# Optimization experiments

Measured on AMD Instinct MI355X. Metric: run time of the kernel, lower is better.

The kernel has to match this reference:

```python
import jax, jax.numpy as jnp
import numpy as np

N_NODES = 50000
N_EDGES = 500000
HID = 256
LAYERS = 15
IN_CH = 2
EPS = 1e-5


def setup_inputs() -> dict:
    key = jax.random.key(0)
    ks = jax.random.split(key, 16)
    s = 0.02
    x = jax.random.normal(ks[0], (N_NODES, IN_CH), dtype=jnp.float32)
    edge_index = jax.random.randint(ks[1], (2, N_EDGES), 0, N_NODES, dtype=jnp.int32)
    # torch-style Linear weights: [out_features, in_features]
    W_in = jax.random.normal(ks[2], (HID, IN_CH), dtype=jnp.float32) * s
    Wrel = jax.random.normal(ks[3], (LAYERS, HID, HID), dtype=jnp.float32) * s
    brel = jnp.zeros((LAYERS, HID), dtype=jnp.float32)
    Wroot = jax.random.normal(ks[4], (LAYERS, HID, HID), dtype=jnp.float32) * s
    gamma = jnp.ones((LAYERS, HID), dtype=jnp.float32)
    beta = jnp.zeros((LAYERS, HID), dtype=jnp.float32)
    W1 = jax.random.normal(ks[5], (HID, 2 * HID), dtype=jnp.float32) * s
    b1 = jnp.zeros((HID,), dtype=jnp.float32)
    W2 = jax.random.normal(ks[6], (HID, HID), dtype=jnp.float32) * s
    b2 = jnp.zeros((HID,), dtype=jnp.float32)
    W3 = jax.random.normal(ks[7], (1, HID), dtype=jnp.float32) * s
    b3 = jnp.zeros((1,), dtype=jnp.float32)
    return {"x": x, "edge_index": edge_index, "W_in": W_in, "Wrel": Wrel,
            "brel": brel, "Wroot": Wroot, "gamma": gamma, "beta": beta,
            "W1": W1, "b1": b1, "W2": W2, "b2": b2, "W3": W3, "b3": b3}


def reference(x, edge_index, W_in, Wrel, brel, Wroot, gamma, beta,
              W1, b1, W2, b2, W3, b3):
    n = x.shape[0]
    src, dst = edge_index[0], edge_index[1]
    h = x @ W_in.T  # input_fc, no bias -> [N, HID]

    def layer(carry, p):
        Wr, br, Wo, g, bt = p
        # GraphConv (aggr='add'): lin_rel(sum_j x_j) + lin_root(x_i)
        agg = jax.ops.segment_sum(carry[src], dst, num_segments=n)
        out = agg @ Wr.T + br + carry @ Wo.T
        # BatchNorm1d, training-mode batch stats (biased var)
        mean = out.mean(axis=0)
        var = out.var(axis=0)
        out = (out - mean) * jax.lax.rsqrt(var + EPS) * g + bt
        return carry + jax.nn.relu(out), None

    h, _ = jax.lax.scan(layer, h, (Wrel, brel, Wroot, gamma, beta))

    # edge MLP on cat([x[row], x[col]])
    e = jnp.concatenate([h[src], h[dst]], axis=-1)  # [E, 2*HID]
    z = jax.nn.relu(e @ W1.T + b1)
    z = jax.nn.relu(z @ W2.T + b2)
    return jax.nn.sigmoid(z @ W3.T + b3)  # [E, 1]
```

## Files before the change

### kernel.cpp

```cpp
#include <hip/hip_runtime.h>
#include <hip/hip_fp8.h>
#include <cstdint>
#include <cstddef>

#define HID 256

typedef __bf16 bf16;
typedef __bf16 bf16x4 __attribute__((ext_vector_type(4)));
typedef __bf16 bf16x8 __attribute__((ext_vector_type(8)));
typedef float f32x4 __attribute__((ext_vector_type(4)));
typedef unsigned char u8;
union f8x8 { uint2 u; u8 b[8]; };

__device__ inline u8 to_fp8(float v) {
  __hip_fp8_e4m3 t(v);
  return t.__x;
}
__device__ inline float from_fp8(u8 b) {
  __hip_fp8_e4m3 t;
  t.__x = b;
  return (float)t;
}


__global__ void k_zero_i32(int* __restrict__ p, int n) {
  int i = blockIdx.x * blockDim.x + threadIdx.x;
  if (i < n) p[i] = 0;
}

__global__ void k_hist(const int* __restrict__ ei, int* __restrict__ deg, int E) {
  int i = blockIdx.x * blockDim.x + threadIdx.x;
  if (i < E) atomicAdd(&deg[ei[E + i]], 1);
}

__global__ void k_scan1(const int* __restrict__ deg, int* __restrict__ offs,
                        int* __restrict__ bsums, int n) {
  __shared__ int sh[1024];
  int i = blockIdx.x * 1024 + threadIdx.x;
  int v = (i < n) ? deg[i] : 0;
  sh[threadIdx.x] = v;
  __syncthreads();
  for (int d = 1; d < 1024; d <<= 1) {
    int t = (threadIdx.x >= (unsigned)d) ? sh[threadIdx.x - d] : 0;
    __syncthreads();
    sh[threadIdx.x] += t;
    __syncthreads();
  }
  if (i < n) offs[i] = sh[threadIdx.x] - v;
  if (threadIdx.x == 1023) bsums[blockIdx.x] = sh[1023];
}

__global__ void k_scan2(int* __restrict__ bsums, int nb) {
  if (threadIdx.x == 0 && blockIdx.x == 0) {
    int run = 0;
    for (int b = 0; b < nb; ++b) { int t = bsums[b]; bsums[b] = run; run += t; }
  }
}

__global__ void k_scan3(int* __restrict__ offs, int* __restrict__ cursor,
                        const int* __restrict__ bsums, int n, int E) {
  int i = blockIdx.x * 1024 + threadIdx.x;
  if (i < n) { int o = offs[i] + bsums[blockIdx.x]; offs[i] = o; cursor[i] = o; }
  if (i == 0) offs[n] = E;
}

__global__ void k_fill(const int* __restrict__ ei, int* __restrict__ cursor,
                       int* __restrict__ csr, int* __restrict__ edst,
                       int* __restrict__ eperm, int E) {
  int i = blockIdx.x * blockDim.x + threadIdx.x;
  if (i < E) {
    int s = ei[i], d = ei[E + i];
    int pos = atomicAdd(&cursor[d], 1);
    csr[pos] = s;
    edst[pos] = d;
    eperm[pos] = i;
  }
}


__global__ void k_pack(const float* __restrict__ W, bf16* __restrict__ P,
                       int OUT, int K, int count) {
  int g = blockIdx.x * blockDim.x + threadIdx.x;
  int total = count * OUT * (K >> 3);
  if (g >= total) return;
  int lane = g & 63;
  int rest = g >> 6;
  int KT = K >> 5;
  int kt = rest % KT;
  int rest2 = rest / KT;
  int OT = OUT >> 4;
  int tile = rest2 % OT;
  int mat = rest2 / OT;
  const float* src = W + (size_t)mat * OUT * K +
                     (size_t)(tile * 16 + (lane & 15)) * K + kt * 32 + (lane >> 4) * 8;
  bf16* dst = P + (size_t)g * 8;
#pragma unroll
  for (int j = 0; j < 8; ++j) dst[j] = (bf16)src[j];
}


__global__ __launch_bounds__(256) void k_input_fc(
    const float* __restrict__ x, const float* __restrict__ Win,
    bf16* __restrict__ hb, u8* __restrict__ h8,
    float* __restrict__ sums0, int N) {
  if (blockIdx.x == 0) { sums0[threadIdx.x] = 0.f; sums0[256 + threadIdx.x] = 0.f; }
  int gid = blockIdx.x * blockDim.x + threadIdx.x;
  int total = N * 32;
  int stride = gridDim.x * blockDim.x;
  for (int idx = gid; idx < total; idx += stride) {
    int node = idx >> 5, c8 = idx & 31;
    float xa = x[2 * node], xb = x[2 * node + 1];
    bf16x8 o;
    f8x8 p;
#pragma unroll
    for (int k = 0; k < 8; ++k) {
      int c = c8 * 8 + k;
      float v = xa * Win[2 * c] + xb * Win[2 * c + 1];
      o[k] = (bf16)v;
      p.b[k] = to_fp8(v);
    }
    *(bf16x8*)(hb + (size_t)node * HID + c8 * 8) = o;
    *(uint2*)(h8 + (size_t)node * HID + c8 * 8) = p.u;
  }
}


__global__ __launch_bounds__(256) void k_aggregate(
    const u8* __restrict__ h8, const int* __restrict__ offs,
    const int* __restrict__ csr, bf16* __restrict__ aggb, int N) {
  int gwave = (int)((blockIdx.x * blockDim.x + threadIdx.x) >> 6);
  int lane = threadIdx.x & 63;
  int node = gwave * 2 + (lane >> 5);
  int l32 = lane & 31;
  if (node >= N) return;
  int e0 = offs[node], e1 = offs[node + 1];
  float a[8] = {};
  int e = e0;
  for (; e + 3 < e1; e += 4) {
    int s0 = csr[e], s1 = csr[e + 1], s2 = csr[e + 2], s3 = csr[e + 3];
    f8x8 p0, p1, p2, p3;
    p0.u = *(const uint2*)(h8 + (size_t)s0 * HID + l32 * 8);
    p1.u = *(const uint2*)(h8 + (size_t)s1 * HID + l32 * 8);
    p2.u = *(const uint2*)(h8 + (size_t)s2 * HID + l32 * 8);
    p3.u = *(const uint2*)(h8 + (size_t)s3 * HID + l32 * 8);
#pragma unroll
    for (int k = 0; k < 8; ++k)
      a[k] += (from_fp8(p0.b[k]) + from_fp8(p1.b[k])) +
              (from_fp8(p2.b[k]) + from_fp8(p3.b[k]));
  }
  for (; e < e1; ++e) {
    int s0 = csr[e];
    f8x8 p0;
    p0.u = *(const uint2*)(h8 + (size_t)s0 * HID + l32 * 8);
#pragma unroll
    for (int k = 0; k < 8; ++k) a[k] += from_fp8(p0.b[k]);
  }
  bf16x8 o;
#pragma unroll
  for (int k = 0; k < 8; ++k) o[k] = (bf16)a[k];
  *(bf16x8*)(aggb + (size_t)node * HID + l32 * 8) = o;
}


__global__ __launch_bounds__(256, 2) void k_layer_gemm(
    const bf16* __restrict__ aggb, const bf16* __restrict__ hb,
    const bf16* __restrict__ Pr, const bf16* __restrict__ Po,
    const float* __restrict__ bias, bf16* __restrict__ out,
    float* __restrict__ sums, int N) {
  __shared__ __align__(16) bf16 bt[64 * 64 * 8];
  __shared__ float bsum[256], bsq[256];
  int tid = threadIdx.x;
  int wave = tid >> 6, lane = tid & 63;
  int l15 = lane & 15, lq = lane >> 4;
  int m0 = blockIdx.x * 128;
  f32x4 acc[4][8] = {};
  const bf16* PrW = Pr + (size_t)wave * 4 * 8 * 64 * 8;
  const bf16* PoW = Po + (size_t)wave * 4 * 8 * 64 * 8;
  int row = tid & 127, half = tid >> 7;
  int sj = row >> 4, sl = row & 15;
  int gr = m0 + row;
  bool ok = gr < N;

  for (int phase = 0; phase < 2; ++phase) {
    const bf16* src = phase ? hb : aggb;
    if (phase) __syncthreads();
    {
#pragma unroll
      for (int i2 = 0; i2 < 16; ++i2) {
        int c = half * 16 + i2;
        bf16x8 v = {};
        if (ok) v = *(const bf16x8*)(src + (size_t)gr * HID + c * 8);
        *(bf16x8*)(&bt[(((c >> 2) * 8 + sj) * 64 + (c & 3) * 16 + sl) * 8]) = v;
      }
    }
    __syncthreads();
    const bf16* PW = phase ? PoW : PrW;
    for (int kt = 0; kt < 8; ++kt) {
      bf16x8 bfr[8];
#pragma unroll
      for (int j = 0; j < 8; ++j)
        bfr[j] = *(const bf16x8*)(&bt[((kt * 8 + j) * 64 + lane) * 8]);
#pragma unroll
      for (int i = 0; i < 4; ++i) {
        bf16x8 afr = *(const bf16x8*)(PW + ((size_t)(i * 8 + kt) * 64 + lane) * 8);
#pragma unroll
        for (int j = 0; j < 8; ++j)
          acc[i][j] = __builtin_amdgcn_mfma_f32_16x16x32_bf16(afr, bfr[j], acc[i][j], 0, 0, 0);
      }
    }
  }

  f32x4 bv[4];
#pragma unroll
  for (int i = 0; i < 4; ++i)
    bv[i] = *(const f32x4*)(bias + wave * 64 + i * 16 + lq * 4);
  float s[4][4] = {}, q[4][4] = {};
#pragma unroll
  for (int j = 0; j < 8; ++j) {
    int gn = m0 + j * 16 + l15;
    bool okj = gn < N;
#pragma unroll
    for (int i = 0; i < 4; ++i) {
      bf16x4 o;
#pragma unroll
      for (int r = 0; r < 4; ++r) {
        float v = acc[i][j][r] + bv[i][r];
        o[r] = (bf16)v;
        if (okj) { s[i][r] += v; q[i][r] += v * v; }
      }
      if (okj) *(bf16x4*)(out + (size_t)gn * HID + wave * 64 + i * 16 + lq * 4) = o;
    }
  }
#pragma unroll
  for (int d = 1; d < 16; d <<= 1) {
#pragma unroll
    for (int i = 0; i < 4; ++i)
#pragma unroll
      for (int r = 0; r < 4; ++r) {
        s[i][r] += __shfl_xor(s[i][r], d, 64);
        q[i][r] += __shfl_xor(q[i][r], d, 64);
      }
  }
  if (l15 == 0) {
#pragma unroll
    for (int i = 0; i < 4; ++i)
#pragma unroll
      for (int r = 0; r < 4; ++r) {
        bsum[wave * 64 + i * 16 + lq * 4 + r] = s[i][r];
        bsq[wave * 64 + i * 16 + lq * 4 + r] = q[i][r];
      }
  }
  __syncthreads();
  atomicAdd(&sums[tid], bsum[tid]);
  atomicAdd(&sums[256 + tid], bsq[tid]);
}


__global__ __launch_bounds__(256) void k_bn_residual(
    const bf16* __restrict__ outb, bf16* __restrict__ hb, u8* __restrict__ h8,
    const float* __restrict__ sums, float* __restrict__ zsums,
    const float* __restrict__ gamma, const float* __restrict__ beta,
    int N, float invN) {
  int t = threadIdx.x;
  if (blockIdx.x == 0) { zsums[t] = 0.f; zsums[256 + t] = 0.f; }
  int cg = (t & 31) * 8;
  int r0 = blockIdx.x * 32 + (t >> 5) * 4;
  float a[8], b[8];
#pragma unroll
  for (int k = 0; k < 8; ++k) {
    int c = cg + k;
    float mean = sums[c] * invN;
    float var = sums[256 + c] * invN - mean * mean;
    float istd = rsqrtf(var + 1e-5f);
    a[k] = istd * gamma[c];
    b[k] = fmaf(-mean, a[k], beta[c]);
  }
  int r1 = min(r0 + 4, N);
  for (int r = r0; r < r1; ++r) {
    size_t idx = (size_t)r * HID + cg;
    bf16x8 ov = *(const bf16x8*)(outb + idx);
    bf16x8 hv = *(const bf16x8*)(hb + idx);
    bf16x8 o;
    f8x8 p;
#pragma unroll
    for (int k = 0; k < 8; ++k) {
      float y = fmaf((float)ov[k], a[k], b[k]);
      y = fmaxf(y, 0.f);
      float hn = (float)hv[k] + y;
      o[k] = (bf16)hn;
      p.b[k] = to_fp8(hn);
    }
    *(bf16x8*)(hb + idx) = o;
    *(uint2*)(h8 + idx) = p.u;
  }
}


__global__ __launch_bounds__(256, 2) void k_edge_mlp(
    const bf16* __restrict__ hb, const int* __restrict__ csr,
    const int* __restrict__ edst, const int* __restrict__ eperm,
    const bf16* __restrict__ P1, const float* __restrict__ b1v,
    const bf16* __restrict__ P2, const float* __restrict__ b2v,
    const float* __restrict__ w3, const float* __restrict__ b3,
    float* __restrict__ outp, int E) {
  __shared__ __align__(16) bf16 z1f[64 * 64 * 8];
  __shared__ int nd[256];
  __shared__ int oidx[128];
  __shared__ float red[128];
  int tid = threadIdx.x;
  int e0 = blockIdx.x * 128;
  {
    int p = e0 + (tid & 127);
    if (tid < 128) {
      nd[tid] = (p < E) ? csr[p] : 0;
      oidx[tid] = (p < E) ? eperm[p] : -1;
      red[tid] = 0.f;
    } else {
      nd[tid] = (p < E) ? edst[p] : 0;
    }
  }
  int wave = tid >> 6, lane = tid & 63;
  int l15 = lane & 15, lq = lane >> 4;
  int row = tid & 127, half = tid >> 7;
  int sslotA = ((row >> 4) * 64 + (half * 2) * 16 + (row & 15)) * 8;
  int sslotB = ((row >> 4) * 64 + (half * 2 + 1) * 16 + (row & 15)) * 8;
  __syncthreads();

  int dnode[8];
#pragma unroll
  for (int j = 0; j < 8; ++j) dnode[j] = nd[128 + j * 16 + l15];

  f32x4 acc[4][8] = {};
  const bf16* P1W = P1 + (size_t)wave * 4 * 16 * 64 * 8;
  {
    int node = nd[row];
    const bf16* rp = hb + (size_t)node * HID + half * 16;
    *(bf16x8*)(&z1f[sslotA]) = *(const bf16x8*)(rp);
    *(bf16x8*)(&z1f[sslotB]) = *(const bf16x8*)(rp + 8);
  }
  __syncthreads();
  for (int ks = 0; ks < 8; ++ks) {
    bf16x8 vn0, vn1;
    bool has = (ks + 1) < 8;
    if (has) {
      int node = nd[row];
      const bf16* rp = hb + (size_t)node * HID + (ks + 1) * 32 + half * 16;
      vn0 = *(const bf16x8*)(rp);
      vn1 = *(const bf16x8*)(rp + 8);
    }
    const bf16* cur = z1f + (ks & 1) * 4096;
    bf16x8 bfr[8];
#pragma unroll
    for (int j = 0; j < 8; ++j)
      bfr[j] = *(const bf16x8*)(&cur[(j * 64 + lane) * 8]);
#pragma unroll
    for (int i = 0; i < 4; ++i) {
      bf16x8 wf = *(const bf16x8*)(P1W + ((size_t)(i * 16 + ks) * 64 + lane) * 8);
#pragma unroll
      for (int j = 0; j < 8; ++j)
        acc[i][j] = __builtin_amdgcn_mfma_f32_16x16x32_bf16(wf, bfr[j], acc[i][j], 0, 0, 0);
    }
    if (has) {
      bf16* nxt = z1f + ((ks + 1) & 1) * 4096;
      *(bf16x8*)(&nxt[sslotA]) = vn0;
      *(bf16x8*)(&nxt[sslotB]) = vn1;
    }
    __syncthreads();
  }

  for (int ks2 = 0; ks2 < 8; ++ks2) {
    bf16x8 bfr[8];
#pragma unroll
    for (int j = 0; j < 8; ++j)
      bfr[j] = *(const bf16x8*)(hb + (size_t)dnode[j] * HID + ks2 * 32 + lq * 8);
#pragma unroll
    for (int i = 0; i < 4; ++i) {
      bf16x8 wf = *(const bf16x8*)(P1W + ((size_t)(i * 16 + 8 + ks2) * 64 + lane) * 8);
#pragma unroll
      for (int j = 0; j < 8; ++j)
        acc[i][j] = __builtin_amdgcn_mfma_f32_16x16x32_bf16(wf, bfr[j], acc[i][j], 0, 0, 0);
    }
  }

  {
    f32x4 b1i[4];
#pragma unroll
    for (int i = 0; i < 4; ++i)
      b1i[i] = *(const f32x4*)(b1v + wave * 64 + i * 16 + lq * 4);
#pragma unroll
    for (int j = 0; j < 8; ++j) {
#pragma unroll
      for (int i = 0; i < 4; ++i) {
        bf16x4 o;
#pragma unroll
        for (int r = 0; r < 4; ++r)
          o[r] = (bf16)fmaxf(acc[i][j][r] + b1i[i][r], 0.f);
        int kt = wave * 2 + (i >> 1);
        int slt = l15 + 16 * ((i & 1) * 2 + (lq >> 1));
        *(bf16x4*)(&z1f[((j * 8 + kt) * 64 + slt) * 8 + (lq & 1) * 4]) = o;
      }
    }
  }
  __syncthreads();

  f32x4 acc2[4][8] = {};
  const bf16* P2W = P2 + (size_t)wave * 4 * 8 * 64 * 8;
  for (int ks = 0; ks < 8; ++ks) {
    bf16x8 zf[8];
#pragma unroll
    for (int j = 0; j < 8; ++j)
      zf[j] = *(const bf16x8*)(&z1f[((j * 8 + ks) * 64 + lane) * 8]);
#pragma unroll
    for (int i = 0; i < 4; ++i) {
      bf16x8 wf = *(const bf16x8*)(P2W + ((size_t)(i * 8 + ks) * 64 + lane) * 8);
#pragma unroll
      for (int j = 0; j < 8; ++j)
        acc2[i][j] = __builtin_amdgcn_mfma_f32_16x16x32_bf16(wf, zf[j], acc2[i][j], 0, 0, 0);
    }
  }

  f32x4 b2i[4], w3i[4];
#pragma unroll
  for (int i = 0; i < 4; ++i) {
    b2i[i] = *(const f32x4*)(b2v + wave * 64 + i * 16 + lq * 4);
    w3i[i] = *(const f32x4*)(w3 + wave * 64 + i * 16 + lq * 4);
  }
  float sj2[8] = {};
#pragma unroll
  for (int j = 0; j < 8; ++j)
#pragma unroll
    for (int i = 0; i < 4; ++i)
#pragma unroll
      for (int r = 0; r < 4; ++r)
        sj2[j] = fmaf(fmaxf(acc2[i][j][r] + b2i[i][r], 0.f), w3i[i][r], sj2[j]);
#pragma unroll
  for (int j = 0; j < 8; ++j) {
    sj2[j] += __shfl_xor(sj2[j], 16, 64);
    sj2[j] += __shfl_xor(sj2[j], 32, 64);
  }
  if (lq == 0) {
#pragma unroll
    for (int j = 0; j < 8; ++j)
      atomicAdd(&red[j * 16 + l15], sj2[j]);
  }
  __syncthreads();
  if (tid < 128) {
    int oi = oidx[tid];
    if (oi >= 0) {
      float logit = red[tid] + b3[0];
      outp[oi] = 1.f / (1.f + expf(-logit));
    }
  }
}


static inline size_t align256(size_t x) { return (x + 255) & ~(size_t)255; }

extern "C" void kernel_launch(void* const* d_in, const int* in_sizes, int n_in,
                              void* d_out, int out_size, void* d_ws, size_t ws_size,
                              hipStream_t stream) {
  const float* x     = (const float*)d_in[0];
  const int*   ei    = (const int*)d_in[1];
  const float* Win   = (const float*)d_in[2];
  const float* Wrel  = (const float*)d_in[3];
  const float* brel  = (const float*)d_in[4];
  const float* Wroot = (const float*)d_in[5];
  const float* gamma = (const float*)d_in[6];
  const float* beta  = (const float*)d_in[7];
  const float* W1    = (const float*)d_in[8];
  const float* b1    = (const float*)d_in[9];
  const float* W2    = (const float*)d_in[10];
  const float* b2    = (const float*)d_in[11];
  const float* W3    = (const float*)d_in[12];
  const float* b3    = (const float*)d_in[13];

  const int N = in_sizes[0] / 2;
  const int E = in_sizes[1] / 2;
  const int L = in_sizes[3] / (HID * HID);

  char* p = (char*)d_ws;
  auto alloc = [&](size_t bytes) { char* r = p; p += align256(bytes); return r; };
  bf16*  hb    = (bf16*)alloc((size_t)N * HID * 2);
  u8*    h8    = (u8*)alloc((size_t)N * HID);
  bf16*  outb  = (bf16*)alloc((size_t)N * HID * 2);
  bf16*  aggb  = (bf16*)alloc((size_t)N * HID * 2);
  bf16*  Prel  = (bf16*)alloc((size_t)L * HID * HID * 2);
  bf16*  Proot = (bf16*)alloc((size_t)L * HID * HID * 2);
  bf16*  P1    = (bf16*)alloc((size_t)HID * 2 * HID * 2);
  bf16*  P2    = (bf16*)alloc((size_t)HID * HID * 2);
  int*   deg   = (int*)alloc((size_t)N * 4);
  int*   offs  = (int*)alloc((size_t)(N + 1) * 4);
  int*   cursor= (int*)alloc((size_t)N * 4);
  int*   csr   = (int*)alloc((size_t)E * 4);
  int*   edst  = (int*)alloc((size_t)E * 4);
  int*   eperm = (int*)alloc((size_t)E * 4);
  int*   bsums = (int*)alloc(64 * 4);
  float* sums  = (float*)alloc(1024 * 4);
  (void)ws_size; (void)n_in; (void)out_size;

  const int nb = (N + 1023) / 1024;

  k_zero_i32<<<(N + 255) / 256, 256, 0, stream>>>(deg, N);
  k_hist<<<(E + 255) / 256, 256, 0, stream>>>(ei, deg, E);
  k_scan1<<<nb, 1024, 0, stream>>>(deg, offs, bsums, N);
  k_scan2<<<1, 64, 0, stream>>>(bsums, nb);
  k_scan3<<<nb, 1024, 0, stream>>>(offs, cursor, bsums, N, E);
  k_fill<<<(E + 255) / 256, 256, 0, stream>>>(ei, cursor, csr, edst, eperm, E);

  {
    int g1 = L * HID * HID / 8;
    k_pack<<<(g1 + 255) / 256, 256, 0, stream>>>(Wrel, Prel, HID, HID, L);
    k_pack<<<(g1 + 255) / 256, 256, 0, stream>>>(Wroot, Proot, HID, HID, L);
    int g2 = HID * 2 * HID / 8;
    k_pack<<<(g2 + 255) / 256, 256, 0, stream>>>(W1, P1, HID, 2 * HID, 1);
    int g3 = HID * HID / 8;
    k_pack<<<(g3 + 255) / 256, 256, 0, stream>>>(W2, P2, HID, HID, 1);
  }

  k_input_fc<<<1024, 256, 0, stream>>>(x, Win, hb, h8, sums, N);

  const float invN = 1.0f / (float)N;
  for (int l = 0; l < L; ++l) {
    int sel = l & 1;
    k_aggregate<<<(N + 7) / 8, 256, 0, stream>>>(h8, offs, csr, aggb, N);
    k_layer_gemm<<<(N + 127) / 128, 256, 0, stream>>>(
        aggb, hb, Prel + (size_t)l * HID * HID, Proot + (size_t)l * HID * HID,
        brel + (size_t)l * HID, outb, sums + sel * 512, N);
    k_bn_residual<<<(N + 31) / 32, 256, 0, stream>>>(
        outb, hb, h8, sums + sel * 512, sums + (1 - sel) * 512,
        gamma + (size_t)l * HID, beta + (size_t)l * HID, N, invN);
  }

  k_edge_mlp<<<(E + 127) / 128, 256, 0, stream>>>(
      hb, csr, edst, eperm, P1, b1, P2, b2, W3, b3, (float*)d_out, E);
}
```

Measured before the change: 1.595 ms.

## Fuse layer GEMM, BatchNorm and residual via cooperative grid sync

Merges the per-layer GEMM and the BatchNorm+ReLU+residual pass into one cooperative kernel. Blocks accumulate channel statistics with atomics, wait at a grid-wide barrier, then normalise their register-resident accumulators and write the bf16 and fp8 copies of h directly. This removes the outb intermediate round trip, the re-read of hb, and one launch per layer. In exchange every block must be co-resident for the grid sync, and the host falls back to the old two-kernel path if the cooperative launch fails.

Result: slower. 2.422 ms (+51.9%).

```diff
diff --git a/kernel.cpp b/kernel.cpp
--- a/kernel.cpp
+++ b/kernel.cpp
@@ -1,9 +1,12 @@
 #include <hip/hip_runtime.h>
+#include <hip/hip_cooperative_groups.h>
 #include <hip/hip_fp8.h>
 #include <cstdint>
 #include <cstddef>
 
 #define HID 256
+
+namespace cg = cooperative_groups;
 
 typedef __bf16 bf16;
 typedef __bf16 bf16x4 __attribute__((ext_vector_type(4)));
@@ -11,6 +14,7 @@
 typedef float f32x4 __attribute__((ext_vector_type(4)));
 typedef unsigned char u8;
 union f8x8 { uint2 u; u8 b[8]; };
+union f8x4 { unsigned int u; u8 b[4]; };
 
 __device__ inline u8 to_fp8(float v) {
   __hip_fp8_e4m3 t(v);
@@ -102,8 +106,11 @@
 __global__ __launch_bounds__(256) void k_input_fc(
     const float* __restrict__ x, const float* __restrict__ Win,
     bf16* __restrict__ hb, u8* __restrict__ h8,
-    float* __restrict__ sums0, int N) {
-  if (blockIdx.x == 0) { sums0[threadIdx.x] = 0.f; sums0[256 + threadIdx.x] = 0.f; }
+    float* __restrict__ sums, int N) {
+  if (blockIdx.x == 0) {
+    sums[threadIdx.x] = 0.f; sums[256 + threadIdx.x] = 0.f;
+    sums[512 + threadIdx.x] = 0.f; sums[768 + threadIdx.x] = 0.f;
+  }
   int gid = blockIdx.x * blockDim.x + threadIdx.x;
   int total = N * 32;
   int stride = gridDim.x * blockDim.x;
@@ -162,6 +169,145 @@
 }
 
 
+
+__global__ __launch_bounds__(256, 2) void k_layer_fused(
+    const bf16* __restrict__ aggb, bf16* __restrict__ hb, u8* __restrict__ h8,
+    const bf16* __restrict__ Pr, const bf16* __restrict__ Po,
+    const float* __restrict__ bias, const float* __restrict__ gamma,
+    const float* __restrict__ beta, float* __restrict__ sums,
+    float* __restrict__ zsums, int N, float invN) {
+  __shared__ __align__(16) bf16 bt[64 * 64 * 8];
+  __shared__ float bsum[256], bsq[256];
+  int tid = threadIdx.x;
+  int wave = tid >> 6, lane = tid & 63;
+  int l15 = lane & 15, lq = lane >> 4;
+  int m0 = blockIdx.x * 128;
+  f32x4 acc[4][8] = {};
+  const bf16* PrW = Pr + (size_t)wave * 4 * 8 * 64 * 8;
+  const bf16* PoW = Po + (size_t)wave * 4 * 8 * 64 * 8;
+  int row = tid & 127, half = tid >> 7;
+  int sj = row >> 4, sl = row & 15;
+  int gr = m0 + row;
+  bool ok = gr < N;
+
+  for (int phase = 0; phase < 2; ++phase) {
+    const bf16* src = phase ? hb : aggb;
+    if (phase) __syncthreads();
+    {
+#pragma unroll
+      for (int i2 = 0; i2 < 16; ++i2) {
+        int c = half * 16 + i2;
+        bf16x8 v = {};
+        if (ok) v = *(const bf16x8*)(src + (size_t)gr * HID + c * 8);
+        *(bf16x8*)(&bt[(((c >> 2) * 8 + sj) * 64 + (c & 3) * 16 + sl) * 8]) = v;
+      }
+    }
+    __syncthreads();
+    const bf16* PW = phase ? PoW : PrW;
+    for (int kt = 0; kt < 8; ++kt) {
+      bf16x8 bfr[8];
+#pragma unroll
+      for (int j = 0; j < 8; ++j)
+        bfr[j] = *(const bf16x8*)(&bt[((kt * 8 + j) * 64 + lane) * 8]);
+#pragma unroll
+      for (int i = 0; i < 4; ++i) {
+        bf16x8 afr = *(const bf16x8*)(PW + ((size_t)(i * 8 + kt) * 64 + lane) * 8);
+#pragma unroll
+        for (int j = 0; j < 8; ++j)
+          acc[i][j] = __builtin_amdgcn_mfma_f32_16x16x32_bf16(afr, bfr[j], acc[i][j], 0, 0, 0);
+      }
+    }
+  }
+
+  f32x4 bv[4];
+#pragma unroll
+  for (int i = 0; i < 4; ++i)
+    bv[i] = *(const f32x4*)(bias + wave * 64 + i * 16 + lq * 4);
+  float s[4][4] = {}, q[4][4] = {};
+#pragma unroll
+  for (int j = 0; j < 8; ++j) {
+    bool okj = (m0 + j * 16 + l15) < N;
+#pragma unroll
+    for (int i = 0; i < 4; ++i) {
+#pragma unroll
+      for (int r = 0; r < 4; ++r) {
+        float v = acc[i][j][r] + bv[i][r];
+        acc[i][j][r] = v;
+        if (okj) { s[i][r] += v; q[i][r] += v * v; }
+      }
+    }
+  }
+#pragma unroll
+  for (int d = 1; d < 16; d <<= 1) {
+#pragma unroll
+    for (int i = 0; i < 4; ++i)
+#pragma unroll
+      for (int r = 0; r < 4; ++r) {
+        s[i][r] += __shfl_xor(s[i][r], d, 64);
+        q[i][r] += __shfl_xor(q[i][r], d, 64);
+      }
+  }
+  if (l15 == 0) {
+#pragma unroll
+    for (int i = 0; i < 4; ++i)
+#pragma unroll
+      for (int r = 0; r < 4; ++r) {
+        bsum[wave * 64 + i * 16 + lq * 4 + r] = s[i][r];
+        bsq[wave * 64 + i * 16 + lq * 4 + r] = q[i][r];
+      }
+  }
+  __syncthreads();
+  atomicAdd(&sums[tid], bsum[tid]);
+  atomicAdd(&sums[256 + tid], bsq[tid]);
+  __threadfence();
+
+  cg::this_grid().sync();
+
+  if (blockIdx.x == 0) { zsums[tid] = 0.f; zsums[256 + tid] = 0.f; }
+
+  float av[4][4], bw[4][4];
+#pragma unroll
+  for (int i = 0; i < 4; ++i) {
+#pragma unroll
+    for (int r = 0; r < 4; ++r) {
+      int ch = wave * 64 + i * 16 + lq * 4 + r;
+      float mean = __hip_atomic_load(&sums[ch], __ATOMIC_RELAXED,
+                                     __HIP_MEMORY_SCOPE_AGENT) * invN;
+      float var = __hip_atomic_load(&sums[256 + ch], __ATOMIC_RELAXED,
+                                    __HIP_MEMORY_SCOPE_AGENT) * invN - mean * mean;
+      float istd = rsqrtf(var + 1e-5f);
+      av[i][r] = istd * gamma[ch];
+      bw[i][r] = fmaf(-mean, av[i][r], beta[ch]);
+    }
+  }
+
+#pragma unroll
+  for (int j = 0; j < 8; ++j) {
+    int gn = m0 + j * 16 + l15;
+    if (gn >= N) continue;
+#pragma unroll
+    for (int i = 0; i < 4; ++i) {
+      int c = wave * 8 + i * 2 + (lq >> 1);
+      bf16x4 hold = *(const bf16x4*)(
+          &bt[(((c >> 2) * 8 + j) * 64 + (c & 3) * 16 + l15) * 8 + (lq & 1) * 4]);
+      bf16x4 o;
+      f8x4 p;
+#pragma unroll
+      for (int r = 0; r < 4; ++r) {
+        float y = fmaf(acc[i][j][r], av[i][r], bw[i][r]);
+        y = fmaxf(y, 0.f);
+        float hn = (float)hold[r] + y;
+        o[r] = (bf16)hn;
+        p.b[r] = to_fp8(hn);
+      }
+      size_t idx = (size_t)gn * HID + wave * 64 + i * 16 + lq * 4;
+      *(bf16x4*)(hb + idx) = o;
+      *(unsigned int*)(h8 + idx) = p.u;
+    }
+  }
+}
+
+
 __global__ __launch_bounds__(256, 2) void k_layer_gemm(
     const bf16* __restrict__ aggb, const bf16* __restrict__ hb,
     const bf16* __restrict__ Pr, const bf16* __restrict__ Po,
@@ -263,12 +409,12 @@
     int N, float invN) {
   int t = threadIdx.x;
   if (blockIdx.x == 0) { zsums[t] = 0.f; zsums[256 + t] = 0.f; }
-  int cg = (t & 31) * 8;
+  int cg2 = (t & 31) * 8;
   int r0 = blockIdx.x * 32 + (t >> 5) * 4;
   float a[8], b[8];
 #pragma unroll
   for (int k = 0; k < 8; ++k) {
-    int c = cg + k;
+    int c = cg2 + k;
     float mean = sums[c] * invN;
     float var = sums[256 + c] * invN - mean * mean;
     float istd = rsqrtf(var + 1e-5f);
@@ -277,7 +423,7 @@
   }
   int r1 = min(r0 + 4, N);
   for (int r = r0; r < r1; ++r) {
-    size_t idx = (size_t)r * HID + cg;
+    size_t idx = (size_t)r * HID + cg2;
     bf16x8 ov = *(const bf16x8*)(outb + idx);
     bf16x8 hv = *(const bf16x8*)(hb + idx);
     bf16x8 o;
@@ -520,15 +666,31 @@
   k_input_fc<<<1024, 256, 0, stream>>>(x, Win, hb, h8, sums, N);
 
   const float invN = 1.0f / (float)N;
+  const int nblk2 = (N + 127) / 128;
   for (int l = 0; l < L; ++l) {
     int sel = l & 1;
     k_aggregate<<<(N + 7) / 8, 256, 0, stream>>>(h8, offs, csr, aggb, N);
-    k_layer_gemm<<<(N + 127) / 128, 256, 0, stream>>>(
-        aggb, hb, Prel + (size_t)l * HID * HID, Proot + (size_t)l * HID * HID,
-        brel + (size_t)l * HID, outb, sums + sel * 512, N);
-    k_bn_residual<<<(N + 31) / 32, 256, 0, stream>>>(
-        outb, hb, h8, sums + sel * 512, sums + (1 - sel) * 512,
-        gamma + (size_t)l * HID, beta + (size_t)l * HID, N, invN);
+
+    const bf16* PrL = Prel + (size_t)l * HID * HID;
+    const bf16* PoL = Proot + (size_t)l * HID * HID;
+    const float* biasL = brel + (size_t)l * HID;
+    const float* gammaL = gamma + (size_t)l * HID;
+    const float* betaL = beta + (size_t)l * HID;
+    float* sumsA = sums + sel * 512;
+    float* sumsB = sums + (1 - sel) * 512;
+    int Nv = N;
+    float invNv = invN;
+    void* args[] = { (void*)&aggb, (void*)&hb, (void*)&h8, (void*)&PrL, (void*)&PoL,
+                     (void*)&biasL, (void*)&gammaL, (void*)&betaL,
+                     (void*)&sumsA, (void*)&sumsB, (void*)&Nv, (void*)&invNv };
+    hipError_t rc = hipLaunchCooperativeKernel(
+        (const void*)k_layer_fused, dim3(nblk2), dim3(256), args, 0, stream);
+    if (rc != hipSuccess) {
+      k_layer_gemm<<<nblk2, 256, 0, stream>>>(
+          aggb, hb, PrL, PoL, biasL, outb, sumsA, N);
+      k_bn_residual<<<(N + 31) / 32, 256, 0, stream>>>(
+          outb, hb, h8, sumsA, sumsB, gammaL, betaL, N, invN);
+    }
   }
 
   k_edge_mlp<<<(E + 127) / 128, 256, 0, stream>>>(
```
